# Kernel optimization log

Hardware: AMD Instinct MI355X
Metric: run time of the kernel (lower is better)

Reference implementation:

```python
import jax, jax.numpy as jnp
import numpy as np

N_NODES = 110
C = 4096  # in_channels = hidden = out_channels


def setup_inputs() -> dict:
    key = jax.random.key(0)
    ks = jax.random.split(key, 8)
    x = jax.random.normal(ks[0], (N_NODES, C), dtype=jnp.float32)
    adj = jax.random.randint(ks[1], (N_NODES, N_NODES), 0, 2, dtype=jnp.int32)
    # torch.nn.Linear weights stored [out_features, in_features]
    W2 = jax.random.normal(ks[2], (C, C), dtype=jnp.float32) / np.sqrt(C)
    b2 = jax.random.normal(ks[3], (C,), dtype=jnp.float32) * 0.01
    W1 = jax.random.normal(ks[4], (2 * C, C), dtype=jnp.float32) / np.sqrt(2 * C)
    b1 = jax.random.normal(ks[5], (C,), dtype=jnp.float32) * 0.01
    Wl = jax.random.normal(ks[6], (N_NODES, N_NODES), dtype=jnp.float32) / np.sqrt(N_NODES)
    bl = jax.random.normal(ks[7], (N_NODES,), dtype=jnp.float32) * 0.01
    # note: W1 is stored [in=2C, out=C]; W2 [in=C, out=C]; Wl [in=110, out=110]
    return {"x": x, "adj": adj, "W2": W2, "b2": b2, "W1": W1, "b1": b1, "Wl": Wl, "bl": bl}


def reference(x, adj, W2, b2, W1, b1, Wl, bl):
    # FeatGraphConv: h = lin2(x)
    h = x @ W2 + b2  # [N, C]
    # edge_index.nonzero(): adjacency -> edge list (i=src, j=dst); mean-aggregate
    # h[src] at dst. Dense equivalent: column-normalized mask matmul.
    mask = (adj != 0).astype(x.dtype)  # [N, N]
    deg = mask.sum(axis=0)  # in-degree of each target node j
    aggr = (mask.T @ h) / jnp.maximum(deg, 1.0)[:, None]  # [N, C]; 0 for isolated nodes (PyG mean)
    # update: lin1(cat(h, aggr)) then relu (in RegGNN.forward)
    out = jax.nn.relu(jnp.concatenate([h, aggr], axis=1) @ W1 + b1)  # [N, C]
    # x.t(); lin(110,110); x.t()
    out = (out.T @ Wl.T + bl).T  # [N, C]
    return out
```

## Files before the change

### kernel.cpp

```cpp
#include <hip/hip_runtime.h>
#include <hip/hip_fp16.h>

#define C 4096
#define NN 110
#define MPAD 112
#define BN 64
#define BK 128
#define KCH 512

typedef _Float16 f16x8 __attribute__((ext_vector_type(8)));
typedef float fx4 __attribute__((ext_vector_type(4)));

#define AS_GLB __attribute__((address_space(1)))
#define AS_LDS __attribute__((address_space(3)))

__global__ void prep1_kernel(const float* __restrict__ x, _Float16* __restrict__ A1) {
    int idx = blockIdx.x * 256 + threadIdx.x;
    int n = idx >> 12;
    float v = (n < NN) ? x[idx] : 0.f;
    A1[idx] = (_Float16)v;
}

__global__ __launch_bounds__(256)
void mm_kernel(const _Float16* __restrict__ A, const float* __restrict__ B,
               float* __restrict__ Cacc, int lda) {
    __shared__ float Bs[2][BK * BN];
    const int t   = threadIdx.x;
    const int w   = t >> 6;
    const int L   = t & 63;
    const int l15 = L & 15;
    const int q   = L >> 4;
    const int n0  = blockIdx.x * BN;
    const int k0  = blockIdx.y * KCH;

    const float* gsrc = B + (size_t)(k0 + w * 32 + (L >> 4)) * C + n0 + (L & 15) * 4;

    auto stage = [&](int buf, int kc) {
        #pragma unroll
        for (int j = 0; j < 8; ++j) {
            const float* g = gsrc + (size_t)(kc + j * 4) * C;
            float* l = &Bs[buf][(w * 32 + j * 4) * BN];
            __builtin_amdgcn_global_load_lds((const AS_GLB void*)g, (AS_LDS void*)l,
                                             16, 0, 0);
        }
    };

    fx4 acc[7];
    #pragma unroll
    for (int mt = 0; mt < 7; ++mt) acc[mt] = (fx4){0.f, 0.f, 0.f, 0.f};

    stage(0, 0);
    #pragma unroll 1
    for (int kc = 0, buf = 0; kc < KCH; kc += BK, buf ^= 1) {
        __syncthreads();
        if (kc + BK < KCH) stage(buf ^ 1, kc + BK);
        const _Float16* Ap = A + (size_t)l15 * lda + k0 + kc + q * 8;
        #pragma unroll
        for (int s = 0; s < 4; ++s) {
            f16x8 bfrag;
            #pragma unroll
            for (int j = 0; j < 8; ++j)
                bfrag[j] = (_Float16)Bs[buf][(s * 32 + q * 8 + j) * BN + w * 16 + l15];
            #pragma unroll
            for (int mt = 0; mt < 7; ++mt) {
                f16x8 afrag = *(const f16x8*)(Ap + (size_t)(mt * 16) * lda + s * 32);
                acc[mt] = __builtin_amdgcn_mfma_f32_16x16x32_f16(afrag, bfrag,
                                                                 acc[mt], 0, 0, 0);
            }
        }
    }

    #pragma unroll
    for (int mt = 0; mt < 7; ++mt) {
        #pragma unroll
        for (int r = 0; r < 4; ++r) {
            int row = mt * 16 + q * 4 + r;
            if (row < NN)
                atomicAdd(&Cacc[(size_t)row * C + n0 + w * 16 + l15], acc[mt][r]);
        }
    }
}

__global__ __launch_bounds__(256)
void agg_kernel(const float* __restrict__ h_raw, const int* __restrict__ adj,
                const float* __restrict__ b2, _Float16* __restrict__ A3) {
    __shared__ float hb[NN * 16];
    __shared__ unsigned long long mlo[NN], mhi[NN];
    __shared__ float degs[NN];
    const int t  = threadIdx.x;
    const int c0 = blockIdx.x * 16;

    for (int idx = t; idx < NN * 16; idx += 256) {
        int n = idx >> 4, c = idx & 15;
        float v = h_raw[(size_t)n * C + c0 + c] + b2[c0 + c];
        hb[idx] = v;
        A3[(size_t)n * (2 * C) + c0 + c] = (_Float16)v;
    }
    if (t < 64) {
        int n  = NN + (t >> 5);
        int hs = (t >> 4) & 1;
        int c  = t & 15;
        A3[(size_t)n * (2 * C) + hs * C + c0 + c] = (_Float16)0.f;
    }
    if (t < NN) {
        int j = t;
        unsigned long long lo = 0, hi = 0;
        int dg = 0;
        for (int i = 0; i < 64; ++i) {
            int m = (adj[i * NN + j] != 0);
            lo |= ((unsigned long long)m) << i; dg += m;
        }
        for (int i = 64; i < NN; ++i) {
            int m = (adj[i * NN + j] != 0);
            hi |= ((unsigned long long)m) << (i - 64); dg += m;
        }
        mlo[j] = lo; mhi[j] = hi;
        degs[j] = (float)(dg > 0 ? dg : 1);
    }
    __syncthreads();
    for (int idx = t; idx < NN * 16; idx += 256) {
        int j = idx >> 4, c = idx & 15;
        unsigned long long lo = mlo[j], hi = mhi[j];
        float a = 0.f;
        #pragma unroll 2
        for (int i = 0; i < 64; ++i)
            a = fmaf((float)((lo >> i) & 1ull), hb[i * 16 + c], a);
        #pragma unroll 2
        for (int i = 64; i < NN; ++i)
            a = fmaf((float)((hi >> (i - 64)) & 1ull), hb[i * 16 + c], a);
        A3[(size_t)j * (2 * C) + C + c0 + c] = (_Float16)(a / degs[j]);
    }
}

__global__ __launch_bounds__(256)
void fin_kernel(const float* __restrict__ z_raw, const float* __restrict__ b1,
                const float* __restrict__ Wl, const float* __restrict__ bl,
                float* __restrict__ out) {
    __shared__ float zs[NN * 64];
    const int t  = threadIdx.x;
    const int c0 = blockIdx.x * 64;
    const int j  = blockIdx.y * 4 + (t >> 6);
    const int c  = t & 63;

    for (int idx = t; idx < NN * 64; idx += 256) {
        int k = idx >> 6, cc = idx & 63;
        float v = z_raw[(size_t)k * C + c0 + cc] + b1[c0 + cc];
        zs[idx] = fmaxf(v, 0.f);
    }
    __syncthreads();
    if (j < NN) {
        float a = bl[j];
        #pragma unroll 2
        for (int k = 0; k < NN; ++k)
            a += Wl[j * NN + k] * zs[k * 64 + c];
        out[(size_t)j * C + c0 + c] = a;
    }
}

extern "C" void kernel_launch(void* const* d_in, const int* in_sizes, int n_in,
                              void* d_out, int out_size, void* d_ws, size_t ws_size,
                              hipStream_t stream) {
    const float* x   = (const float*)d_in[0];
    const int*   adj = (const int*)d_in[1];
    const float* W2  = (const float*)d_in[2];
    const float* b2  = (const float*)d_in[3];
    const float* W1  = (const float*)d_in[4];
    const float* b1  = (const float*)d_in[5];
    const float* Wl  = (const float*)d_in[6];
    const float* bl  = (const float*)d_in[7];
    float* out = (float*)d_out;

    char* ws = (char*)d_ws;
    float*    h_raw = (float*)(ws);
    float*    z_raw = (float*)(ws + 1802240);
    _Float16* A1    = (_Float16*)(ws + 3604480);
    _Float16* A3    = (_Float16*)(ws + 4521984);

    hipMemsetAsync(d_ws, 0, 3604480, stream);
    prep1_kernel<<<(MPAD * C) / 256, 256, 0, stream>>>(x, A1);
    mm_kernel<<<dim3(C / BN, C / KCH), 256, 0, stream>>>(A1, W2, h_raw, C);
    agg_kernel<<<C / 16, 256, 0, stream>>>(h_raw, adj, b2, A3);
    mm_kernel<<<dim3(C / BN, (2 * C) / KCH), 256, 0, stream>>>(A3, W1, z_raw, 2 * C);
    fin_kernel<<<dim3(C / 64, 28), 256, 0, stream>>>(z_raw, b1, Wl, bl, out);
}
```

Baseline: 386.2 us.

## Widen GEMM N-tile, stage A in LDS, and rebalance split-K grid

Restructures the skinny GEMM so each block covers 256 output columns, with each wave computing a 7x4 grid of MFMA tiles. A fragments are now staged once per K-step in shared memory and reused across four B sub-tiles, where before they were reloaded from global memory per wave. Split-K becomes a runtime parameter giving 32 K-chunks for both GEMMs. The change drops double-buffering of B in favour of a single buffer with two barriers per step, which risks exposing load latency, and it raises register pressure with 28 accumulators.

```diff
diff --git a/kernel.cpp b/kernel.cpp
--- a/kernel.cpp
+++ b/kernel.cpp
@@ -4,11 +4,12 @@
 #define C 4096
 #define NN 110
 #define MPAD 112
-#define BN 64
-#define BK 128
-#define KCH 512
+#define BN 256
+#define BK 32
+#define ASTR 40
 
 typedef _Float16 f16x8 __attribute__((ext_vector_type(8)));
+typedef _Float16 f16x4 __attribute__((ext_vector_type(4)));
 typedef float fx4 __attribute__((ext_vector_type(4)));
 
 #define AS_GLB __attribute__((address_space(1)))
@@ -21,62 +22,75 @@
     A1[idx] = (_Float16)v;
 }
 
-__global__ __launch_bounds__(256)
+__global__ __launch_bounds__(256, 2)
 void mm_kernel(const _Float16* __restrict__ A, const float* __restrict__ B,
-               float* __restrict__ Cacc, int lda) {
-    __shared__ float Bs[2][BK * BN];
+               float* __restrict__ Cacc, int lda, int kch) {
+    __shared__ float    Bs[BK * BN];
+    __shared__ _Float16 As[MPAD * ASTR];
+
     const int t   = threadIdx.x;
     const int w   = t >> 6;
     const int L   = t & 63;
     const int l15 = L & 15;
     const int q   = L >> 4;
     const int n0  = blockIdx.x * BN;
-    const int k0  = blockIdx.y * KCH;
+    const int k0  = blockIdx.y * kch;
 
-    const float* gsrc = B + (size_t)(k0 + w * 32 + (L >> 4)) * C + n0 + (L & 15) * 4;
+    fx4 acc[7][4];
+    #pragma unroll
+    for (int mt = 0; mt < 7; ++mt)
+        #pragma unroll
+        for (int nt = 0; nt < 4; ++nt)
+            acc[mt][nt] = (fx4){0.f, 0.f, 0.f, 0.f};
 
-    auto stage = [&](int buf, int kc) {
+    #pragma unroll 1
+    for (int kc = 0; kc < kch; kc += BK) {
         #pragma unroll
         for (int j = 0; j < 8; ++j) {
-            const float* g = gsrc + (size_t)(kc + j * 4) * C;
-            float* l = &Bs[buf][(w * 32 + j * 4) * BN];
-            __builtin_amdgcn_global_load_lds((const AS_GLB void*)g, (AS_LDS void*)l,
-                                             16, 0, 0);
+            const int row = w * 8 + j;
+            const float* g = B + (size_t)(k0 + kc + row) * C + n0 + L * 4;
+            __builtin_amdgcn_global_load_lds((const AS_GLB void*)g,
+                                             (AS_LDS void*)(Bs + row * BN), 16, 0, 0);
         }
-    };
-
-    fx4 acc[7];
-    #pragma unroll
-    for (int mt = 0; mt < 7; ++mt) acc[mt] = (fx4){0.f, 0.f, 0.f, 0.f};
-
-    stage(0, 0);
-    #pragma unroll 1
-    for (int kc = 0, buf = 0; kc < KCH; kc += BK, buf ^= 1) {
+        #pragma unroll
+        for (int i = 0; i < 4; ++i) {
+            int idx = t + i * 256;
+            if (idx < MPAD * 8) {
+                int row = idx >> 3;
+                int c4  = (idx & 7) * 4;
+                f16x4 v = *(const f16x4*)(A + (size_t)row * lda + k0 + kc + c4);
+                *(f16x4*)(As + row * ASTR + c4) = v;
+            }
+        }
         __syncthreads();
-        if (kc + BK < KCH) stage(buf ^ 1, kc + BK);
-        const _Float16* Ap = A + (size_t)l15 * lda + k0 + kc + q * 8;
+        f16x8 bfrag[4];
         #pragma unroll
-        for (int s = 0; s < 4; ++s) {
-            f16x8 bfrag;
+        for (int nt = 0; nt < 4; ++nt)
             #pragma unroll
             for (int j = 0; j < 8; ++j)
-                bfrag[j] = (_Float16)Bs[buf][(s * 32 + q * 8 + j) * BN + w * 16 + l15];
+                bfrag[nt][j] = (_Float16)Bs[(q * 8 + j) * BN + w * 64 + nt * 16 + l15];
+        #pragma unroll
+        for (int mt = 0; mt < 7; ++mt) {
+            f16x8 af = *(const f16x8*)(As + (mt * 16 + l15) * ASTR + q * 8);
             #pragma unroll
-            for (int mt = 0; mt < 7; ++mt) {
-                f16x8 afrag = *(const f16x8*)(Ap + (size_t)(mt * 16) * lda + s * 32);
-                acc[mt] = __builtin_amdgcn_mfma_f32_16x16x32_f16(afrag, bfrag,
-                                                                 acc[mt], 0, 0, 0);
-            }
+            for (int nt = 0; nt < 4; ++nt)
+                acc[mt][nt] = __builtin_amdgcn_mfma_f32_16x16x32_f16(af, bfrag[nt],
+                                                                     acc[mt][nt], 0, 0, 0);
         }
+        __syncthreads();
     }
 
     #pragma unroll
     for (int mt = 0; mt < 7; ++mt) {
         #pragma unroll
-        for (int r = 0; r < 4; ++r) {
-            int row = mt * 16 + q * 4 + r;
-            if (row < NN)
-                atomicAdd(&Cacc[(size_t)row * C + n0 + w * 16 + l15], acc[mt][r]);
+        for (int nt = 0; nt < 4; ++nt) {
+            const int col = n0 + w * 64 + nt * 16 + l15;
+            #pragma unroll
+            for (int r = 0; r < 4; ++r) {
+                int row = mt * 16 + q * 4 + r;
+                if (row < NN)
+                    atomicAdd(&Cacc[(size_t)row * C + col], acc[mt][nt][r]);
+            }
         }
     }
 }
@@ -178,8 +192,8 @@
 
     hipMemsetAsync(d_ws, 0, 3604480, stream);
     prep1_kernel<<<(MPAD * C) / 256, 256, 0, stream>>>(x, A1);
-    mm_kernel<<<dim3(C / BN, C / KCH), 256, 0, stream>>>(A1, W2, h_raw, C);
+    mm_kernel<<<dim3(C / BN, 32), 256, 0, stream>>>(A1, W2, h_raw, C, 128);
     agg_kernel<<<C / 16, 256, 0, stream>>>(h_raw, adj, b2, A3);
-    mm_kernel<<<dim3(C / BN, (2 * C) / KCH), 256, 0, stream>>>(A3, W1, z_raw, 2 * C);
+    mm_kernel<<<dim3(C / BN, 32), 256, 0, stream>>>(A3, W1, z_raw, 2 * C, 256);
     fin_kernel<<<dim3(C / 64, 28), 256, 0, stream>>>(z_raw, b1, Wl, bl, out);
 }
```

Result: slower. 414.9 us (+7.4%).
